# Optimization experiments

Measured on AMD Instinct MI355X. Metric: run time of the kernel, lower is better.

Reference implementation:

```python
import jax, jax.numpy as jnp
import numpy as np

BN_EPS = 1e-3  # Keras BatchNormalization default epsilon


def _conv_block(x, k):
    """Per-task conv (stride 2, pad 1) -> ReLU -> BatchNorm (center/scale=False, training).

    x: [B, E, H, W, Cin]  (B tasks, E examples per task)
    k: [B, kh, kw, Cin, Cout]  per-task kernel
    """
    def conv_one(xe, kt):  # xe: [E,H,W,Cin], kt: [kh,kw,Cin,Cout]
        return jax.lax.conv_general_dilated(
            xe, kt, window_strides=(2, 2), padding=[(1, 1), (1, 1)],
            dimension_numbers=('NHWC', 'HWIO', 'NHWC'))
    y = jax.nn.relu(jax.vmap(conv_one)(x, k))  # [B,E,H',W',Cout]
    # BatchNorm in training mode: moments over all axes except channels
    m = jnp.mean(y, axis=(0, 1, 2, 3))
    v = jnp.var(y, axis=(0, 1, 2, 3))
    return (y - m) * jax.lax.rsqrt(v + BN_EPS)


def setup_inputs() -> dict:
    key = jax.random.key(0)
    ks = jax.random.split(key, 6)
    B, E, H, C, O = 64, 64, 28, 64, 20
    return {
        'x': jax.random.normal(ks[0], (B, E, H, H, 1), dtype=jnp.float32),
        'k1': jax.random.normal(ks[1], (B, 3, 3, 1, C), dtype=jnp.float32) * 0.1,
        'k2': jax.random.normal(ks[2], (B, 3, 3, C, C), dtype=jnp.float32) * 0.05,
        'k3': jax.random.normal(ks[3], (B, 3, 3, C, C), dtype=jnp.float32) * 0.05,
        'k4': jax.random.normal(ks[4], (B, 3, 3, C, C), dtype=jnp.float32) * 0.05,
        'w_ro': jax.random.normal(ks[5], (B, C, O), dtype=jnp.float32) * 0.1,
    }


def reference(x, k1, k2, k3, k4, w_ro):
    h = _conv_block(x, k1)   # [B,E,14,14,C]
    h = _conv_block(h, k2)   # [B,E,7,7,C]
    h = _conv_block(h, k3)   # [B,E,4,4,C]
    h = _conv_block(h, k4)   # [B,E,2,2,C]
    # MaxPooling2D with pool size == full spatial extent -> global spatial max
    feat = jnp.max(h, axis=(2, 3))  # [B,E,C]
    # per-task readout matmul: [B,E,H] x [B,H,O] -> [B,E,O]
    return jnp.einsum('beh,bho->beo', feat, w_ro)
```

## Files before the change

kernel.cpp:

```cpp
#include <hip/hip_runtime.h>

#define BN_EPS 1e-3f

typedef __attribute__((ext_vector_type(8))) short bf16x8;
typedef __attribute__((ext_vector_type(16))) float floatx16;
typedef unsigned short u16;

__device__ __forceinline__ u16 f2bf(float f) {
  unsigned u = __float_as_uint(f);
  u += 0x7fffu + ((u >> 16) & 1u);
  return (u16)(u >> 16);
}
__device__ __forceinline__ float bf2f(u16 h) {
  return __uint_as_float(((unsigned)h) << 16);
}

static constexpr int NSHARD = 256;

__global__ __launch_bounds__(256) void conv1_kernel(
    const float* __restrict__ x, const float* __restrict__ k1,
    u16* __restrict__ y1, float* __restrict__ statsSh)
{
  __shared__ float xp[900];
  __shared__ float w1[576];
  __shared__ float red[256];

  const int be = blockIdx.x, b = be >> 6, tid = threadIdx.x;

  for (int i = tid; i < 900; i += 256) xp[i] = 0.f;
  for (int i = tid; i < 576; i += 256) w1[i] = k1[(size_t)b * 576 + i];
  __syncthreads();
  for (int i = tid; i < 784; i += 256) {
    const int r = i / 28, cc = i - 28 * r;
    xp[(r + 1) * 30 + (cc + 1)] = x[(size_t)be * 784 + i];
  }
  __syncthreads();

  const int c = tid & 63;
  float wr[9];
#pragma unroll
  for (int t = 0; t < 9; ++t) wr[t] = w1[t * 64 + c];

  float sum = 0.f, ss = 0.f;
  for (int pix = tid >> 6; pix < 196; pix += 4) {
    const int oy = pix / 14, ox = pix - 14 * oy;
    const float* xb = &xp[(2 * oy) * 30 + 2 * ox];
    float acc = 0.f;
#pragma unroll
    for (int ky = 0; ky < 3; ++ky)
#pragma unroll
      for (int kx = 0; kx < 3; ++kx)
        acc = fmaf(xb[ky * 30 + kx], wr[ky * 3 + kx], acc);
    const float v = fmaxf(acc, 0.f);
    y1[((size_t)be * 196 + pix) * 64 + c] = f2bf(v);
    sum += v;
    ss = fmaf(v, v, ss);
  }

  red[tid] = sum;
  __syncthreads();
  if (tid < 64)
    atomicAdd(&statsSh[(blockIdx.x & (NSHARD - 1)) * 128 + tid],
              red[tid] + red[tid + 64] + red[tid + 128] + red[tid + 192]);
  __syncthreads();
  red[tid] = ss;
  __syncthreads();
  if (tid < 64)
    atomicAdd(&statsSh[(blockIdx.x & (NSHARD - 1)) * 128 + 64 + tid],
              red[tid] + red[tid + 64] + red[tid + 128] + red[tid + 192]);
}

__global__ __launch_bounds__(256) void fold_kernel(
    const float* __restrict__ W, const float* __restrict__ statsSh, float invN,
    u16* __restrict__ Wf, float* __restrict__ biasCls)
{
  __shared__ float T[64 * 68];
  __shared__ float P[256];
  __shared__ float s1[64], t1[64];
  __shared__ float TB[576];

  const int b = blockIdx.x, tid = threadIdx.x;

  {
    const int g = tid >> 7, cidx = tid & 127;
    float acc = 0.f;
    for (int k = 0; k < 128; ++k) acc += statsSh[(g * 128 + k) * 128 + cidx];
    P[tid] = acc;
  }
  __syncthreads();
  if (tid < 128) T[tid] = P[tid] + P[tid + 128];
  __syncthreads();
  if (tid < 64) {
    const float m = T[tid] * invN;
    const float var = fmaf(-m, m, T[64 + tid] * invN);
    const float s = rsqrtf(var + BN_EPS);
    s1[tid] = s;
    t1[tid] = -m * s;
  }
  for (int i = tid; i < 576; i += 256) TB[i] = 0.f;
  __syncthreads();

  const int cin = tid >> 2, q0 = (tid & 3) * 16;
  const int cout = tid >> 2, ci0 = (tid & 3) * 16;
  for (int s = 0; s < 9; ++s) {
    const float* ss = W + ((size_t)b * 9 + s) * 4096;
#pragma unroll
    for (int q = 0; q < 16; q += 4) {
      const float4 v = *(const float4*)(ss + cin * 64 + q0 + q);
      T[(q0 + q + 0) * 68 + cin] = v.x;
      T[(q0 + q + 1) * 68 + cin] = v.y;
      T[(q0 + q + 2) * 68 + cin] = v.z;
      T[(q0 + q + 3) * 68 + cin] = v.w;
    }
    __syncthreads();
    alignas(16) u16 tmp[16];
    float tb = 0.f;
#pragma unroll
    for (int j = 0; j < 16; ++j) {
      const float wv = T[cout * 68 + ci0 + j];
      tmp[j] = f2bf(wv * s1[ci0 + j]);
      tb = fmaf(t1[ci0 + j], wv, tb);
    }
    u16* dst = Wf + ((size_t)b * 9 + s) * 4096 + cout * 64 + ci0;
    *(uint4*)dst       = *(uint4*)&tmp[0];
    *(uint4*)(dst + 8) = *(uint4*)&tmp[8];
    atomicAdd(&TB[s * 64 + cout], tb);
    __syncthreads();
  }

  for (int idx = tid; idx < 576; idx += 256) {
    const int cls = idx >> 6, cc = idx & 63;
    const int ry = cls / 3, rx = cls % 3;
    float bsum = 0.f;
#pragma unroll
    for (int s = 0; s < 9; ++s) {
      const int ky = s / 3, kx = s % 3;
      const bool valid = !((ry == 1 && ky == 0) || (ry == 2 && ky == 2) ||
                           (rx == 1 && kx == 0) || (rx == 2 && kx == 2));
      if (valid) bsum += TB[s * 64 + cc];
    }
    biasCls[(size_t)b * 576 + idx] = bsum;
  }
}

template <int Hin, int Hout, int G>
__global__ __launch_bounds__(256) void conv_gemm_kernel(
    const u16* __restrict__ yin, const u16* __restrict__ Wf,
    const float* __restrict__ biasCls, u16* __restrict__ yout,
    float* __restrict__ statsSh)
{
  constexpr int PPI  = Hout * Hout;
  constexpr int ROWS = G * PPI;
  constexpr int BPT  = 64 / G;

  __shared__ __align__(16) u16 AS[64 * 72];
  __shared__ __align__(16) u16 BtS[64 * 72];
  __shared__ float biasS[576];
  __shared__ float redsum[64], redss[64];

  const int b = blockIdx.x / BPT;
  const int e0 = (blockIdx.x % BPT) * G;
  const int tid = threadIdx.x, lane = tid & 63, wave = tid >> 6;

  for (int i = tid; i < 576; i += 256) biasS[i] = biasCls[(size_t)b * 576 + i];
  if (tid < 64) { redsum[tid] = 0.f; redss[tid] = 0.f; }

  const int row = tid >> 2, ci0 = (tid & 3) * 16;
  const int e_l = row / PPI, pp = row % PPI;
  const int oy = pp / Hout, ox = pp % Hout;
  const bool rowOk = row < ROWS;
  const size_t inBase = ((size_t)(b * 64 + e0 + e_l)) * (Hin * Hin) * 64;

  const int mi = wave & 1, ni = wave >> 1;
  const int m0 = mi * 32, n0 = ni * 32;
  const int arow = m0 + (lane & 31), kq = (lane >> 5) * 8;

  floatx16 acc;
#pragma unroll
  for (int r = 0; r < 16; ++r) acc[r] = 0.f;

  __syncthreads();

#pragma unroll
  for (int s = 0; s < 9; ++s) {
    const int ky = s / 3, kx = s % 3;
    const int iy = 2 * oy - 1 + ky, ix = 2 * ox - 1 + kx;
    const bool ok = rowOk && ((unsigned)iy < (unsigned)Hin) &&
                    ((unsigned)ix < (unsigned)Hin);
    uint4 v0 = {0, 0, 0, 0}, v1 = {0, 0, 0, 0};
    if (ok) {
      const u16* src = yin + inBase + (size_t)(iy * Hin + ix) * 64 + ci0;
      v0 = *(const uint4*)src;
      v1 = *(const uint4*)(src + 8);
    }
    *(uint4*)&AS[row * 72 + ci0]     = v0;
    *(uint4*)&AS[row * 72 + ci0 + 8] = v1;
    {
      const u16* g = Wf + ((size_t)b * 9 + s) * 4096 + row * 64 + ci0;
      *(uint4*)&BtS[row * 72 + ci0]     = *(const uint4*)g;
      *(uint4*)&BtS[row * 72 + ci0 + 8] = *(const uint4*)(g + 8);
    }
    __syncthreads();
    const u16* ap = &AS[arow * 72 + kq];
    const u16* bp = &BtS[(n0 + (lane & 31)) * 72 + kq];
#pragma unroll
    for (int st = 0; st < 4; ++st) {
      bf16x8 af = *(const bf16x8*)(ap + st * 16);
      bf16x8 bv = *(const bf16x8*)(bp + st * 16);
      acc = __builtin_amdgcn_mfma_f32_32x32x16_bf16(af, bv, acc, 0, 0, 0);
    }
    __syncthreads();
  }

  const int col = n0 + (lane & 31);
  const int rbase = m0 + 4 * (lane >> 5);
  float ls = 0.f, lss = 0.f;
#pragma unroll
  for (int r = 0; r < 16; ++r) {
    const int rw = rbase + (r & 3) + 8 * (r >> 2);
    if (rw < ROWS) {
      const int re = rw / PPI, pr = rw % PPI;
      const int ooy = pr / Hout, oox = pr % Hout;
      const int ry = (ooy == 0) ? 1 : ((2 * ooy + 1 >= Hin) ? 2 : 0);
      const int rx = (oox == 0) ? 1 : ((2 * oox + 1 >= Hin) ? 2 : 0);
      const float v = fmaxf(acc[r] + biasS[(ry * 3 + rx) * 64 + col], 0.f);
      yout[((size_t)(b * 64 + e0 + re) * PPI + pr) * 64 + col] = f2bf(v);
      ls += v;
      lss = fmaf(v, v, lss);
    }
  }
  atomicAdd(&redsum[col], ls);
  atomicAdd(&redss[col], lss);
  __syncthreads();
  if (tid < 64) {
    const int sh = blockIdx.x & (NSHARD - 1);
    atomicAdd(&statsSh[sh * 128 + tid], redsum[tid]);
    atomicAdd(&statsSh[sh * 128 + 64 + tid], redss[tid]);
  }
}

__global__ __launch_bounds__(256) void readout_kernel(
    const u16* __restrict__ y4, const float* __restrict__ w_ro,
    const float* __restrict__ statsSh, float invN, float* __restrict__ outp)
{
  __shared__ float wl[64 * 20];
  __shared__ float feat[64 * 64];
  __shared__ float P[256];
  __shared__ float sArr[64], tArr[64];

  const int b = blockIdx.x, tid = threadIdx.x;

  {
    const int g = tid >> 7, cidx = tid & 127;
    float acc = 0.f;
    for (int k = 0; k < 128; ++k) acc += statsSh[(g * 128 + k) * 128 + cidx];
    P[tid] = acc;
  }
  for (int i = tid; i < 1280; i += 256) wl[i] = w_ro[(size_t)b * 1280 + i];
  __syncthreads();
  if (tid < 64) {
    const float m = (P[tid] + P[tid + 128]) * invN;
    const float var = fmaf(-m, m, (P[64 + tid] + P[192 + tid]) * invN);
    const float s = rsqrtf(var + BN_EPS);
    sArr[tid] = s;
    tArr[tid] = -m * s;
  }
  __syncthreads();

  {
    const int e = tid & 63;
    for (int c = tid >> 6; c < 64; c += 4) {
      const u16* p4 = y4 + ((size_t)(b * 64 + e) * 4) * 64 + c;
      const float v = fmaxf(fmaxf(bf2f(p4[0]), bf2f(p4[64])),
                            fmaxf(bf2f(p4[128]), bf2f(p4[192])));
      feat[c * 64 + e] = fmaf(v, sArr[c], tArr[c]);
    }
  }
  __syncthreads();

  const int e = tid >> 2, og = (tid & 3) * 5;
  float acc[5] = {0.f, 0.f, 0.f, 0.f, 0.f};
  for (int c = 0; c < 64; ++c) {
    const float f = feat[c * 64 + e];
#pragma unroll
    for (int j = 0; j < 5; ++j) acc[j] = fmaf(f, wl[c * 20 + og + j], acc[j]);
  }
#pragma unroll
  for (int j = 0; j < 5; ++j)
    outp[((size_t)b * 64 + e) * 20 + og + j] = acc[j];
}

extern "C" void kernel_launch(void* const* d_in, const int* in_sizes, int n_in,
                              void* d_out, int out_size, void* d_ws, size_t ws_size,
                              hipStream_t stream) {
  (void)in_sizes; (void)n_in; (void)out_size; (void)ws_size;
  const float* x   = (const float*)d_in[0];
  const float* k1  = (const float*)d_in[1];
  const float* k2  = (const float*)d_in[2];
  const float* k3  = (const float*)d_in[3];
  const float* k4  = (const float*)d_in[4];
  const float* wro = (const float*)d_in[5];
  float* out = (float*)d_out;
  char* ws = (char*)d_ws;

  float* stats = (float*)ws;
  u16* k2f = (u16*)(ws + 524288);
  u16* k3f = k2f + (size_t)2359296;
  u16* k4f = k3f + (size_t)2359296;
  float* bias2 = (float*)(ws + 524288 + 3 * (size_t)4718592);
  float* bias3 = bias2 + 36864;
  float* bias4 = bias3 + 36864;
  u16* y2 = (u16*)((char*)(bias4 + 36864));
  u16* y1 = y2 + (size_t)12845056;
  u16* y3 = y1;
  u16* y4 = y3 + (size_t)4194304;

  float* st1 = stats;
  float* st2 = stats + 32768;
  float* st3 = stats + 65536;
  float* st4 = stats + 98304;

  hipMemsetAsync(stats, 0, 524288, stream);

  conv1_kernel<<<4096, 256, 0, stream>>>(x, k1, y1, st1);
  fold_kernel<<<64, 256, 0, stream>>>(k2, st1, 1.f / 802816.f, k2f, bias2);
  conv_gemm_kernel<14, 7, 1><<<4096, 256, 0, stream>>>(y1, k2f, bias2, y2, st2);
  fold_kernel<<<64, 256, 0, stream>>>(k3, st2, 1.f / 200704.f, k3f, bias3);
  conv_gemm_kernel<7, 4, 4><<<1024, 256, 0, stream>>>(y2, k3f, bias3, y3, st3);
  fold_kernel<<<64, 256, 0, stream>>>(k4, st3, 1.f / 65536.f, k4f, bias4);
  conv_gemm_kernel<4, 2, 16><<<256, 256, 0, stream>>>(y3, k4f, bias4, y4, st4);
  readout_kernel<<<64, 256, 0, stream>>>(y4, wro, st4, 1.f / 16384.f, out);
}
```

Before: 268.1 us.

## Enlarge conv GEMM tile to 256 rows and split fold across three blocks

The conv GEMM kernel now gives each block 256 output rows, and each wave computes a 64x64 tile with four MFMA accumulators. This reuses each staged weight tile across four times as many rows and quarters the grid size. The fold kernel is split into three blocks per task, each handling three taps. Its bias classes are accumulated with global atomics into a zeroed region, which means the memset now also covers the bias buffers. The trade-off is fewer blocks for the later layers (only 64 blocks for layer 4), more register pressure from four accumulators, and more LDS use.

```diff
diff --git a/kernel.cpp b/kernel.cpp
--- a/kernel.cpp
+++ b/kernel.cpp
@@ -77,9 +77,10 @@
   __shared__ float T[64 * 68];
   __shared__ float P[256];
   __shared__ float s1[64], t1[64];
-  __shared__ float TB[576];
-
-  const int b = blockIdx.x, tid = threadIdx.x;
+  __shared__ float tbS[64];
+
+  const int b = blockIdx.x / 3, sg = blockIdx.x % 3;
+  const int tid = threadIdx.x;
 
   {
     const int g = tid >> 7, cidx = tid & 127;
@@ -88,21 +89,19 @@
     P[tid] = acc;
   }
   __syncthreads();
-  if (tid < 128) T[tid] = P[tid] + P[tid + 128];
-  __syncthreads();
   if (tid < 64) {
-    const float m = T[tid] * invN;
-    const float var = fmaf(-m, m, T[64 + tid] * invN);
+    const float m = (P[tid] + P[tid + 128]) * invN;
+    const float var = fmaf(-m, m, (P[64 + tid] + P[192 + tid]) * invN);
     const float s = rsqrtf(var + BN_EPS);
     s1[tid] = s;
     t1[tid] = -m * s;
   }
-  for (int i = tid; i < 576; i += 256) TB[i] = 0.f;
   __syncthreads();
 
   const int cin = tid >> 2, q0 = (tid & 3) * 16;
   const int cout = tid >> 2, ci0 = (tid & 3) * 16;
-  for (int s = 0; s < 9; ++s) {
+  for (int s = sg * 3; s < sg * 3 + 3; ++s) {
+    if (tid < 64) tbS[tid] = 0.f;
     const float* ss = W + ((size_t)b * 9 + s) * 4096;
 #pragma unroll
     for (int q = 0; q < 16; q += 4) {
@@ -124,22 +123,20 @@
     u16* dst = Wf + ((size_t)b * 9 + s) * 4096 + cout * 64 + ci0;
     *(uint4*)dst       = *(uint4*)&tmp[0];
     *(uint4*)(dst + 8) = *(uint4*)&tmp[8];
-    atomicAdd(&TB[s * 64 + cout], tb);
-    __syncthreads();
-  }
-
-  for (int idx = tid; idx < 576; idx += 256) {
-    const int cls = idx >> 6, cc = idx & 63;
-    const int ry = cls / 3, rx = cls % 3;
-    float bsum = 0.f;
-#pragma unroll
-    for (int s = 0; s < 9; ++s) {
+    atomicAdd(&tbS[cout], tb);
+    __syncthreads();
+    if (tid < 64) {
       const int ky = s / 3, kx = s % 3;
-      const bool valid = !((ry == 1 && ky == 0) || (ry == 2 && ky == 2) ||
-                           (rx == 1 && kx == 0) || (rx == 2 && kx == 2));
-      if (valid) bsum += TB[s * 64 + cc];
-    }
-    biasCls[(size_t)b * 576 + idx] = bsum;
+      const float tv = tbS[tid];
+#pragma unroll
+      for (int cls = 0; cls < 9; ++cls) {
+        const int ry = cls / 3, rx = cls % 3;
+        const bool valid = !((ry == 1 && ky == 0) || (ry == 2 && ky == 2) ||
+                             (rx == 1 && kx == 0) || (rx == 2 && kx == 2));
+        if (valid) atomicAdd(&biasCls[(size_t)b * 576 + cls * 64 + tid], tv);
+      }
+    }
+    __syncthreads();
   }
 }
 
@@ -153,7 +150,7 @@
   constexpr int ROWS = G * PPI;
   constexpr int BPT  = 64 / G;
 
-  __shared__ __align__(16) u16 AS[64 * 72];
+  __shared__ __align__(16) u16 AS[256 * 72];
   __shared__ __align__(16) u16 BtS[64 * 72];
   __shared__ float biasS[576];
   __shared__ float redsum[64], redss[64];
@@ -165,72 +162,95 @@
   for (int i = tid; i < 576; i += 256) biasS[i] = biasCls[(size_t)b * 576 + i];
   if (tid < 64) { redsum[tid] = 0.f; redss[tid] = 0.f; }
 
-  const int row = tid >> 2, ci0 = (tid & 3) * 16;
-  const int e_l = row / PPI, pp = row % PPI;
+  const int row = tid;
+  const bool rowOk = row < ROWS;
+  const int g = rowOk ? row / PPI : 0;
+  const int pp = rowOk ? row % PPI : 0;
   const int oy = pp / Hout, ox = pp % Hout;
-  const bool rowOk = row < ROWS;
-  const size_t inBase = ((size_t)(b * 64 + e0 + e_l)) * (Hin * Hin) * 64;
-
-  const int mi = wave & 1, ni = wave >> 1;
-  const int m0 = mi * 32, n0 = ni * 32;
-  const int arow = m0 + (lane & 31), kq = (lane >> 5) * 8;
-
-  floatx16 acc;
-#pragma unroll
-  for (int r = 0; r < 16; ++r) acc[r] = 0.f;
-
-  __syncthreads();
+  const size_t inBase = ((size_t)(b * 64 + e0 + g)) * (Hin * Hin) * 64;
+
+  if (!rowOk) {
+#pragma unroll
+    for (int j = 0; j < 8; ++j) *(uint4*)&AS[row * 72 + j * 8] = uint4{0, 0, 0, 0};
+  }
+
+  const int bco = tid >> 2, bci = (tid & 3) * 16;
+
+  const int m0 = wave * 64;
+  const int l31 = lane & 31;
+  const int kq = (lane >> 5) * 8;
+
+  floatx16 acc00, acc01, acc10, acc11;
+#pragma unroll
+  for (int r = 0; r < 16; ++r) { acc00[r] = 0.f; acc01[r] = 0.f; acc10[r] = 0.f; acc11[r] = 0.f; }
 
 #pragma unroll
   for (int s = 0; s < 9; ++s) {
     const int ky = s / 3, kx = s % 3;
-    const int iy = 2 * oy - 1 + ky, ix = 2 * ox - 1 + kx;
-    const bool ok = rowOk && ((unsigned)iy < (unsigned)Hin) &&
-                    ((unsigned)ix < (unsigned)Hin);
-    uint4 v0 = {0, 0, 0, 0}, v1 = {0, 0, 0, 0};
-    if (ok) {
-      const u16* src = yin + inBase + (size_t)(iy * Hin + ix) * 64 + ci0;
-      v0 = *(const uint4*)src;
-      v1 = *(const uint4*)(src + 8);
-    }
-    *(uint4*)&AS[row * 72 + ci0]     = v0;
-    *(uint4*)&AS[row * 72 + ci0 + 8] = v1;
+    if (rowOk) {
+      const int iy = 2 * oy - 1 + ky, ix = 2 * ox - 1 + kx;
+      const bool ok = ((unsigned)iy < (unsigned)Hin) && ((unsigned)ix < (unsigned)Hin);
+      if (ok) {
+        const u16* src = yin + inBase + (size_t)(iy * Hin + ix) * 64;
+#pragma unroll
+        for (int j = 0; j < 8; ++j)
+          *(uint4*)&AS[row * 72 + j * 8] = *(const uint4*)(src + j * 8);
+      } else {
+#pragma unroll
+        for (int j = 0; j < 8; ++j) *(uint4*)&AS[row * 72 + j * 8] = uint4{0, 0, 0, 0};
+      }
+    }
     {
-      const u16* g = Wf + ((size_t)b * 9 + s) * 4096 + row * 64 + ci0;
-      *(uint4*)&BtS[row * 72 + ci0]     = *(const uint4*)g;
-      *(uint4*)&BtS[row * 72 + ci0 + 8] = *(const uint4*)(g + 8);
-    }
-    __syncthreads();
-    const u16* ap = &AS[arow * 72 + kq];
-    const u16* bp = &BtS[(n0 + (lane & 31)) * 72 + kq];
-#pragma unroll
-    for (int st = 0; st < 4; ++st) {
-      bf16x8 af = *(const bf16x8*)(ap + st * 16);
-      bf16x8 bv = *(const bf16x8*)(bp + st * 16);
-      acc = __builtin_amdgcn_mfma_f32_32x32x16_bf16(af, bv, acc, 0, 0, 0);
-    }
-    __syncthreads();
-  }
-
-  const int col = n0 + (lane & 31);
-  const int rbase = m0 + 4 * (lane >> 5);
-  float ls = 0.f, lss = 0.f;
-#pragma unroll
-  for (int r = 0; r < 16; ++r) {
-    const int rw = rbase + (r & 3) + 8 * (r >> 2);
-    if (rw < ROWS) {
-      const int re = rw / PPI, pr = rw % PPI;
-      const int ooy = pr / Hout, oox = pr % Hout;
-      const int ry = (ooy == 0) ? 1 : ((2 * ooy + 1 >= Hin) ? 2 : 0);
-      const int rx = (oox == 0) ? 1 : ((2 * oox + 1 >= Hin) ? 2 : 0);
-      const float v = fmaxf(acc[r] + biasS[(ry * 3 + rx) * 64 + col], 0.f);
-      yout[((size_t)(b * 64 + e0 + re) * PPI + pr) * 64 + col] = f2bf(v);
-      ls += v;
-      lss = fmaf(v, v, lss);
-    }
-  }
-  atomicAdd(&redsum[col], ls);
-  atomicAdd(&redss[col], lss);
+      const u16* gw = Wf + ((size_t)b * 9 + s) * 4096 + bco * 64 + bci;
+      *(uint4*)&BtS[bco * 72 + bci]     = *(const uint4*)gw;
+      *(uint4*)&BtS[bco * 72 + bci + 8] = *(const uint4*)(gw + 8);
+    }
+    __syncthreads();
+#pragma unroll
+    for (int kk = 0; kk < 4; ++kk) {
+      const int ko = kk * 16 + kq;
+      bf16x8 a0 = *(const bf16x8*)&AS[(m0 + l31) * 72 + ko];
+      bf16x8 a1 = *(const bf16x8*)&AS[(m0 + 32 + l31) * 72 + ko];
+      bf16x8 b0 = *(const bf16x8*)&BtS[l31 * 72 + ko];
+      bf16x8 b1 = *(const bf16x8*)&BtS[(32 + l31) * 72 + ko];
+      acc00 = __builtin_amdgcn_mfma_f32_32x32x16_bf16(a0, b0, acc00, 0, 0, 0);
+      acc01 = __builtin_amdgcn_mfma_f32_32x32x16_bf16(a0, b1, acc01, 0, 0, 0);
+      acc10 = __builtin_amdgcn_mfma_f32_32x32x16_bf16(a1, b0, acc10, 0, 0, 0);
+      acc11 = __builtin_amdgcn_mfma_f32_32x32x16_bf16(a1, b1, acc11, 0, 0, 0);
+    }
+    __syncthreads();
+  }
+
+  float ls0 = 0.f, lss0 = 0.f, ls1 = 0.f, lss1 = 0.f;
+  const int col0 = l31, col1 = 32 + l31;
+  const int rb = m0 + 4 * (lane >> 5);
+#pragma unroll
+  for (int mt = 0; mt < 2; ++mt) {
+    const floatx16& aN0 = mt ? acc10 : acc00;
+    const floatx16& aN1 = mt ? acc11 : acc01;
+#pragma unroll
+    for (int r = 0; r < 16; ++r) {
+      const int rw = rb + mt * 32 + (r & 3) + 8 * (r >> 2);
+      if (rw < ROWS) {
+        const int re = rw / PPI, pr = rw % PPI;
+        const int ooy = pr / Hout, oox = pr % Hout;
+        const int ry = (ooy == 0) ? 1 : ((2 * ooy + 1 >= Hin) ? 2 : 0);
+        const int rx = (oox == 0) ? 1 : ((2 * oox + 1 >= Hin) ? 2 : 0);
+        const int cls = ry * 3 + rx;
+        const size_t ob = ((size_t)(b * 64 + e0 + re) * PPI + pr) * 64;
+        const float v0 = fmaxf(aN0[r] + biasS[cls * 64 + col0], 0.f);
+        const float v1 = fmaxf(aN1[r] + biasS[cls * 64 + col1], 0.f);
+        yout[ob + col0] = f2bf(v0);
+        yout[ob + col1] = f2bf(v1);
+        ls0 += v0; lss0 = fmaf(v0, v0, lss0);
+        ls1 += v1; lss1 = fmaf(v1, v1, lss1);
+      }
+    }
+  }
+  atomicAdd(&redsum[col0], ls0);
+  atomicAdd(&redss[col0], lss0);
+  atomicAdd(&redsum[col1], ls1);
+  atomicAdd(&redss[col1], lss1);
   __syncthreads();
   if (tid < 64) {
     const int sh = blockIdx.x & (NSHARD - 1);
@@ -304,13 +324,13 @@
   char* ws = (char*)d_ws;
 
   float* stats = (float*)ws;
-  u16* k2f = (u16*)(ws + 524288);
+  float* bias2 = (float*)(ws + 524288);
+  float* bias3 = bias2 + 36864;
+  float* bias4 = bias3 + 36864;
+  u16* k2f = (u16*)(ws + 524288 + 442368);
   u16* k3f = k2f + (size_t)2359296;
   u16* k4f = k3f + (size_t)2359296;
-  float* bias2 = (float*)(ws + 524288 + 3 * (size_t)4718592);
-  float* bias3 = bias2 + 36864;
-  float* bias4 = bias3 + 36864;
-  u16* y2 = (u16*)((char*)(bias4 + 36864));
+  u16* y2 = k4f + (size_t)2359296;
   u16* y1 = y2 + (size_t)12845056;
   u16* y3 = y1;
   u16* y4 = y3 + (size_t)4194304;
@@ -320,14 +340,14 @@
   float* st3 = stats + 65536;
   float* st4 = stats + 98304;
 
-  hipMemsetAsync(stats, 0, 524288, stream);
+  hipMemsetAsync(stats, 0, 524288 + 442368, stream);
 
   conv1_kernel<<<4096, 256, 0, stream>>>(x, k1, y1, st1);
-  fold_kernel<<<64, 256, 0, stream>>>(k2, st1, 1.f / 802816.f, k2f, bias2);
-  conv_gemm_kernel<14, 7, 1><<<4096, 256, 0, stream>>>(y1, k2f, bias2, y2, st2);
-  fold_kernel<<<64, 256, 0, stream>>>(k3, st2, 1.f / 200704.f, k3f, bias3);
-  conv_gemm_kernel<7, 4, 4><<<1024, 256, 0, stream>>>(y2, k3f, bias3, y3, st3);
-  fold_kernel<<<64, 256, 0, stream>>>(k4, st3, 1.f / 65536.f, k4f, bias4);
-  conv_gemm_kernel<4, 2, 16><<<256, 256, 0, stream>>>(y3, k4f, bias4, y4, st4);
+  fold_kernel<<<192, 256, 0, stream>>>(k2, st1, 1.f / 802816.f, k2f, bias2);
+  conv_gemm_kernel<14, 7, 4><<<1024, 256, 0, stream>>>(y1, k2f, bias2, y2, st2);
+  fold_kernel<<<192, 256, 0, stream>>>(k3, st2, 1.f / 200704.f, k3f, bias3);
+  conv_gemm_kernel<7, 4, 16><<<256, 256, 0, stream>>>(y2, k3f, bias3, y3, st3);
+  fold_kernel<<<192, 256, 0, stream>>>(k4, st3, 1.f / 65536.f, k4f, bias4);
+  conv_gemm_kernel<4, 2, 64><<<64, 256, 0, stream>>>(y3, k4f, bias4, y4, st4);
   readout_kernel<<<64, 256, 0, stream>>>(y4, wro, st4, 1.f / 16384.f, out);
 }
```

Result: no change. 270.4 us (+0.9%).
